# Optimization experiments

Hardware: AMD Instinct MI355X
Metric: run time of the kernel (lower is better)

The kernel has to match this reference:

```python
import jax, jax.numpy as jnp
import numpy as np

B = 32; N_NODES = 1000; WINDOW = 4; D = 128; N_PARTS = 10
T = 2; T_INT = 1; T_TEMP = 1
N_TOTAL = B * WINDOW * N_NODES
E_INT = 200000; E_TEMP = 96000


def setup_inputs() -> dict:
    key = jax.random.key(0)
    ks = jax.random.split(key, 24)
    inp = {}
    inp["node_inputs"] = jax.random.randint(ks[0], (B, N_NODES), 0, 10)
    inp["node_indices"] = jax.random.randint(ks[1], (E_INT,), 0, N_TOTAL)
    inp["neighbour_indices"] = jax.random.randint(ks[2], (E_INT,), 0, N_TOTAL)
    inp["temp_node_indices"] = jax.random.randint(ks[3], (E_TEMP,), 0, N_TOTAL)
    inp["temp_neighbour_indices"] = jax.random.randint(ks[4], (E_TEMP,), 0, N_TOTAL)

    def dense(k, din, dout):
        return jax.random.normal(k, (din, dout), jnp.float32) * np.float32(1.0 / np.sqrt(din))

    inp["embed_table"] = jax.random.normal(ks[5], (10, D), jnp.float32)
    # message MLP: 2*D -> 64 -> 64 -> 64 -> 64 -> D (4 gelu hidden, linear out)
    inp["msg_W_in"] = dense(ks[6], 2 * D, 64); inp["msg_b_in"] = jnp.zeros((64,), jnp.float32)
    inp["msg_W_hid"] = jax.random.normal(ks[7], (3, 64, 64), jnp.float32) * np.float32(1.0 / 8.0)
    inp["msg_b_hid"] = jnp.zeros((3, 64), jnp.float32)
    inp["msg_W_out"] = dense(ks[8], 64, D); inp["msg_b_out"] = jnp.zeros((D,), jnp.float32)
    # readout MLP: D -> 64 -> 64 -> 64 -> 64 -> n_parts
    inp["ro_W_in"] = dense(ks[9], D, 64); inp["ro_b_in"] = jnp.zeros((64,), jnp.float32)
    inp["ro_W_hid"] = jax.random.normal(ks[10], (3, 64, 64), jnp.float32) * np.float32(1.0 / 8.0)
    inp["ro_b_hid"] = jnp.zeros((3, 64), jnp.float32)
    inp["ro_W_out"] = dense(ks[11], 64, N_PARTS); inp["ro_b_out"] = jnp.zeros((N_PARTS,), jnp.float32)
    # GRU cells (tf.keras reset_after=True): kernel [D,3D], recurrent [D,3D], input+recurrent biases
    for nm, base in (("gi", 12), ("gt", 16)):
        inp[nm + "_Wx"] = dense(ks[base], D, 3 * D)
        inp[nm + "_Wh"] = dense(ks[base + 1], D, 3 * D)
        inp[nm + "_bi"] = jnp.zeros((3 * D,), jnp.float32)
        inp[nm + "_br"] = jnp.zeros((3 * D,), jnp.float32)
    return inp


def _mlp(x, W_in, b_in, W_hid, b_hid, W_out, b_out):
    h = jax.nn.gelu(x @ W_in + b_in, approximate=False)
    for i in range(W_hid.shape[0]):
        h = jax.nn.gelu(h @ W_hid[i] + b_hid[i], approximate=False)
    return h @ W_out + b_out


def _gru(h, x, Wx, Wh, bi, br):
    # tf.keras GRUCell, reset_after=True
    xz, xr, xh = jnp.split(x @ Wx + bi, 3, axis=1)
    hz, hr, hh = jnp.split(h @ Wh + br, 3, axis=1)
    z = jax.nn.sigmoid(xz + hz)
    r = jax.nn.sigmoid(xr + hr)
    cand = jnp.tanh(xh + r * hh)
    return z * h + (1.0 - z) * cand


def _message_mean(h, ni, bi, msg_p):
    g0 = h[ni]              # [E, D] node gather
    g1 = h[bi]              # [E, D] neighbour gather
    x = jnp.concatenate([jnp.concatenate([g0, g1], 1), jnp.concatenate([g1, g0], 1)], 0)  # [2E, 2D]
    msg = _mlp(x, *msg_p)   # [2E, D]
    seg = jnp.concatenate([bi, ni], 0)
    s = jax.ops.segment_sum(msg, seg, num_segments=h.shape[0])
    c = jax.ops.segment_sum(jnp.ones((seg.shape[0], 1), msg.dtype), seg, num_segments=h.shape[0])
    return s / jnp.maximum(c, 1.0)


def reference(node_inputs, node_indices, neighbour_indices, temp_node_indices, temp_neighbour_indices,
              embed_table, msg_W_in, msg_b_in, msg_W_hid, msg_b_hid, msg_W_out, msg_b_out,
              ro_W_in, ro_b_in, ro_W_hid, ro_b_hid, ro_W_out, ro_b_out,
              gi_Wx, gi_Wh, gi_bi, gi_br, gt_Wx, gt_Wh, gt_bi, gt_br):
    msg_p = (msg_W_in, msg_b_in, msg_W_hid, msg_b_hid, msg_W_out, msg_b_out)
    h = embed_table[node_inputs]                       # [B, N, D]
    h = jnp.repeat(h, WINDOW, axis=0).reshape(-1, D)   # [B*W*N, D]
    for _ in range(T):
        for _ in range(T_INT):
            m = _message_mean(h, node_indices, neighbour_indices, msg_p)
            h = _gru(h, m, gi_Wx, gi_Wh, gi_bi, gi_br)
        for _ in range(T_TEMP):
            m = _message_mean(h, temp_node_indices, temp_neighbour_indices, msg_p)
            h = _gru(h, m, gt_Wx, gt_Wh, gt_bi, gt_br)
    ridx = jnp.arange(N_NODES)[None, :] + jnp.arange(B)[:, None] * (WINDOW * N_NODES)
    return _mlp(h[ridx], ro_W_in, ro_b_in, ro_W_hid, ro_b_hid, ro_W_out, ro_b_out)  # [B, N, n_parts]
```

## Files before the change

### kernel.cpp

```cpp
#include <hip/hip_runtime.h>
#include <math.h>


#define DDIM 128
#define NTOT 128000
#define HBYTES 65536000ULL
#define EBLK 128

typedef unsigned short u16;
using f32x4 = __attribute__((ext_vector_type(4))) float;
using s16x8 = __attribute__((ext_vector_type(8))) short;

__device__ __forceinline__ float fast_rcp(float x) {
    return __builtin_amdgcn_rcpf(x);
}
__device__ __forceinline__ float gelu_fast(float x) {
    const float ax = fabsf(x) * 0.70710678118654752440f;
    const float t  = fast_rcp(1.0f + 0.3275911f * ax);
    const float poly = t * (0.254829592f + t * (-0.284496736f +
                       t * (1.421413741f + t * (-1.453152027f +
                       t * 1.061405429f))));
    const float e = __expf(-ax * ax);
    const float erfax = 1.0f - poly * e;
    const float erfv = copysignf(erfax, x);
    return 0.5f * x * (1.0f + erfv);
}
__device__ __forceinline__ float sigmoid_fast(float x) {
    return fast_rcp(1.0f + __expf(-x));
}
__device__ __forceinline__ float tanh_fast(float x) {
    const float e = __expf(2.0f * x);
    return 1.0f - 2.0f * fast_rcp(e + 1.0f);
}
__device__ __forceinline__ u16 f2bf(float x) {
    unsigned u = __float_as_uint(x);
    u += 0x7fffu + ((u >> 16) & 1u);
    return (u16)(u >> 16);
}
__device__ __forceinline__ float bf2f(u16 h) {
    return __uint_as_float(((unsigned)h) << 16);
}

__global__ __launch_bounds__(256) void embed_kernel(
    const int* __restrict__ inp, const float* __restrict__ table,
    float* __restrict__ h)
{
    int gid = blockIdx.x * 256 + threadIdx.x;
    if (gid >= NTOT * 32) return;
    int row = gid >> 5;
    int q   = gid & 31;
    int b   = row / 4000;
    int n   = (row % 4000) % 1000;
    int e   = inp[b * 1000 + n];
    ((float4*)h)[gid] = ((const float4*)table)[e * 32 + q];
}

__global__ __launch_bounds__(256) void hist_kernel(
    const int* __restrict__ ni, const int* __restrict__ bi, int E,
    int* __restrict__ deg)
{
    int g = blockIdx.x * 256 + threadIdx.x;
    if (g < E)          atomicAdd(&deg[bi[g]], 1);
    else if (g < 2 * E) atomicAdd(&deg[ni[g - E]], 1);
}

__global__ __launch_bounds__(256) void blockscan_kernel(
    const int* __restrict__ deg, int* __restrict__ offp, int* __restrict__ bsum)
{
    __shared__ int s[256];
    int tid = threadIdx.x;
    int i = blockIdx.x * 256 + tid;
    int v = deg[i];
    s[tid] = v;
    __syncthreads();
    for (int off = 1; off < 256; off <<= 1) {
        int t = (tid >= off) ? s[tid - off] : 0;
        __syncthreads();
        s[tid] += t;
        __syncthreads();
    }
    offp[i] = s[tid] - v;
    if (tid == 255) bsum[blockIdx.x] = s[255];
}

__global__ __launch_bounds__(512) void bscan_kernel(
    const int* __restrict__ bsum, int* __restrict__ bexc, int nb)
{
    __shared__ int s[512];
    int t = threadIdx.x;
    int v = (t < nb) ? bsum[t] : 0;
    s[t] = v;
    __syncthreads();
    for (int off = 1; off < 512; off <<= 1) {
        int u = (t >= off) ? s[t - off] : 0;
        __syncthreads();
        s[t] += u;
        __syncthreads();
    }
    if (t < nb) bexc[t] = s[t] - v;
}

__global__ __launch_bounds__(256) void fill_kernel(
    const int* __restrict__ ni, const int* __restrict__ bi, int E,
    const int* __restrict__ offp, const int* __restrict__ bexc,
    int* __restrict__ cursor, int* __restrict__ elist, int* __restrict__ slotseg)
{
    int g = blockIdx.x * 256 + threadIdx.x;
    if (g >= 2 * E) return;
    int seg = (g < E) ? bi[g] : ni[g - E];
    int pos = atomicAdd(&cursor[seg], 1);
    int slot = offp[seg] + bexc[seg >> 8] + pos;
    elist[slot] = g;
    slotseg[slot] = seg;
}

__global__ __launch_bounds__(256) void straddle_kernel(
    const int* __restrict__ slotseg, int nblocks32,
    int* __restrict__ list, int* __restrict__ count)
{
    int b = blockIdx.x * 256 + threadIdx.x + 1;
    if (b >= nblocks32) return;
    int s = slotseg[b * 32];
    if (s >= 0 && slotseg[b * 32 - 1] == s) {
        int pos = atomicAdd(count, 1);
        list[pos] = s;
    }
}

__global__ __launch_bounds__(64) void zero_rows_kernel(
    const int* __restrict__ list, const int* __restrict__ count,
    float* __restrict__ sbuf)
{
    int i = blockIdx.x;
    if (i >= *count) return;
    int seg = list[i];
    float4* row = (float4*)(sbuf + (size_t)seg * 64);
    if (threadIdx.x < 16) row[threadIdx.x] = make_float4(0.f, 0.f, 0.f, 0.f);
}

__global__ __launch_bounds__(256) void pack_gateB_kernel(
    const float* __restrict__ Wx, const float* __restrict__ Wh,
    u16* __restrict__ BH, u16* __restrict__ BL)
{
    int idx = blockIdx.x * 256 + threadIdx.x;
    if (idx >= 131072) return;
    int j    = idx & 7;
    int lane = (idx >> 3) & 63;
    int ntG  = (idx >> 9) & 31;
    int ktG  = idx >> 14;
    int k = ktG * 32 + (lane >> 4) * 8 + j;
    int n = ntG * 16 + (lane & 15);
    int g = n >> 7, jj = n & 127;
    float v;
    if (g == 0)      v = (k < 128) ? Wx[k * 384 + jj]       : Wh[(k - 128) * 384 + jj];
    else if (g == 1) v = (k < 128) ? Wx[k * 384 + 128 + jj] : Wh[(k - 128) * 384 + 128 + jj];
    else if (g == 2) v = (k < 128) ? Wx[k * 384 + 256 + jj] : 0.0f;
    else             v = (k < 128) ? 0.0f                   : Wh[(k - 128) * 384 + 256 + jj];
    u16 hb = f2bf(v);
    BH[idx] = hb;
    BL[idx] = f2bf(v - bf2f(hb));
}

__global__ __launch_bounds__(256) void pack_preB_kernel(
    const float* __restrict__ Win, u16* __restrict__ BH, u16* __restrict__ BL)
{
    int idx = blockIdx.x * 256 + threadIdx.x;
    if (idx >= 16384) return;
    int j    = idx & 7;
    int lane = (idx >> 3) & 63;
    int nt2  = (idx >> 9) & 7;
    int kt2  = idx >> 12;
    int k = kt2 * 32 + (lane >> 4) * 8 + j;
    int n = nt2 * 16 + (lane & 15);
    float v = (n < 64) ? Win[k * 64 + n] : Win[(128 + k) * 64 + (n - 64)];
    u16 hb = f2bf(v);
    BH[idx] = hb;
    BL[idx] = f2bf(v - bf2f(hb));
}

__global__ __launch_bounds__(256) void pack_hidB_kernel(
    const float* __restrict__ Whid, u16* __restrict__ BH, u16* __restrict__ BL)
{
    int idx = blockIdx.x * 256 + threadIdx.x;
    if (idx >= 12288) return;
    int j    = idx & 7;
    int lane = (idx >> 3) & 63;
    int nt   = (idx >> 9) & 3;
    int kt   = (idx >> 11) & 1;
    int L    = idx >> 12;
    int k = kt * 32 + (lane >> 4) * 8 + j;
    int n = nt * 16 + (lane & 15);
    float v = Whid[L * 4096 + k * 64 + n];
    u16 hb = f2bf(v);
    BH[idx] = hb;
    BL[idx] = f2bf(v - bf2f(hb));
}

__global__ __launch_bounds__(256) void pack_outB_kernel(
    const float* __restrict__ Wout, u16* __restrict__ BH, u16* __restrict__ BL)
{
    int idx = blockIdx.x * 256 + threadIdx.x;
    if (idx >= 8192) return;
    int j    = idx & 7;
    int lane = (idx >> 3) & 63;
    int nt   = (idx >> 9) & 7;
    int kt   = idx >> 12;
    int k = kt * 32 + (lane >> 4) * 8 + j;
    int n = nt * 16 + (lane & 15);
    float v = Wout[k * 128 + n];
    u16 hb = f2bf(v);
    BH[idx] = hb;
    BL[idx] = f2bf(v - bf2f(hb));
}

__global__ __launch_bounds__(512, 2) void node_pre_mfma(
    const float* __restrict__ h,
    const u16* __restrict__ BpH, const u16* __restrict__ BpL,
    const float* __restrict__ binp, float* __restrict__ pout)
{
    __shared__ short sm[32768];
    const int tid  = threadIdx.x;
    const int lane = tid & 63;
    const int w    = tid >> 6;
    const int jg   = w & 1;
    const int mh   = w >> 1;
    const int nbase = blockIdx.x * 128;

    const int mS = tid >> 2, q = tid & 3;
    const int nodeS = nbase + mS;
    const int laneS = (mS & 15) + 16 * q;
    const int seg_m = mS >> 4;

    #pragma unroll
    for (int c = 0; c < 4; ++c) {
        const int kl = c * 32 + q * 8;
        const float* src = h + (size_t)nodeS * DDIM + kl;
        const float4 v0 = ((const float4*)src)[0];
        const float4 v1 = ((const float4*)src)[1];
        float xv[8] = { v0.x, v0.y, v0.z, v0.w, v1.x, v1.y, v1.z, v1.w };
        s16x8 hi8, lo8;
        #pragma unroll
        for (int i = 0; i < 8; ++i) {
            u16 hb = f2bf(xv[i]);
            hi8[i] = (short)hb;
            lo8[i] = (short)f2bf(xv[i] - bf2f(hb));
        }
        const int off = (c * 8 + seg_m) * 512 + laneS * 8;
        *(s16x8*)(sm + off)         = hi8;
        *(s16x8*)(sm + off + 16384) = lo8;
    }
    __syncthreads();

    f32x4 acc2[2][4];
    #pragma unroll
    for (int mf = 0; mf < 2; ++mf)
        #pragma unroll
        for (int t4 = 0; t4 < 4; ++t4)
            acc2[mf][t4] = (f32x4){0.f, 0.f, 0.f, 0.f};

    const s16x8* Ph8 = (const s16x8*)BpH;
    const s16x8* Pl8 = (const s16x8*)BpL;
    #pragma unroll
    for (int kt2 = 0; kt2 < 4; ++kt2) {
        const int a0off = (kt2 * 8 + 2 * mh) * 512 + lane * 8;
        const s16x8 aH0 = *(const s16x8*)(sm + a0off);
        const s16x8 aL0 = *(const s16x8*)(sm + 16384 + a0off);
        const s16x8 aH1 = *(const s16x8*)(sm + a0off + 512);
        const s16x8 aL1 = *(const s16x8*)(sm + 16384 + a0off + 512);
        #pragma unroll
        for (int t4 = 0; t4 < 4; ++t4) {
            const int idx = (kt2 * 8 + jg * 4 + t4) * 64 + lane;
            const s16x8 bH = Ph8[idx];
            const s16x8 bL = Pl8[idx];
            acc2[0][t4] = __builtin_amdgcn_mfma_f32_16x16x32_bf16(aH0, bH, acc2[0][t4], 0, 0, 0);
            acc2[0][t4] = __builtin_amdgcn_mfma_f32_16x16x32_bf16(aH0, bL, acc2[0][t4], 0, 0, 0);
            acc2[0][t4] = __builtin_amdgcn_mfma_f32_16x16x32_bf16(aL0, bH, acc2[0][t4], 0, 0, 0);
            acc2[1][t4] = __builtin_amdgcn_mfma_f32_16x16x32_bf16(aH1, bH, acc2[1][t4], 0, 0, 0);
            acc2[1][t4] = __builtin_amdgcn_mfma_f32_16x16x32_bf16(aH1, bL, acc2[1][t4], 0, 0, 0);
            acc2[1][t4] = __builtin_amdgcn_mfma_f32_16x16x32_bf16(aL1, bH, acc2[1][t4], 0, 0, 0);
        }
    }
    #pragma unroll
    for (int mf = 0; mf < 2; ++mf) {
        const int mtile = 2 * mh + mf;
        #pragma unroll
        for (int t4 = 0; t4 < 4; ++t4) {
            const int n = jg * 64 + t4 * 16 + (lane & 15);
            const float badd = (n < 64) ? binp[n] : 0.0f;
            #pragma unroll
            for (int r = 0; r < 4; ++r) {
                const int m = mtile * 16 + (lane >> 4) * 4 + r;
                pout[(size_t)(nbase + m) * DDIM + n] = acc2[mf][t4][r] + badd;
            }
        }
    }
}

__global__ __launch_bounds__(512) void edge_mlp_mfma(
    const int* __restrict__ ni, const int* __restrict__ bi, int E,
    const int* __restrict__ elist, const int* __restrict__ slotseg,
    const float* __restrict__ p,
    const u16* __restrict__ BhH, const u16* __restrict__ BhL,
    const float* __restrict__ bhid,
    float* __restrict__ sbuf)
{
    __shared__ short smA[17408];
    __shared__ int   segLDS[EBLK];
    __shared__ int   segedge[2];
    float* scat = (float*)smA;

    const int tid  = threadIdx.x;
    const int lane = tid & 63;
    const int w    = tid >> 6;
    const int s0   = blockIdx.x * EBLK;

    if (tid < 128) segLDS[tid] = slotseg[s0 + tid];
    if (tid == 0) segedge[0] = slotseg[s0 - 1];
    if (tid == 1) segedge[1] = slotseg[s0 + EBLK];

    {
        const int m  = (tid & 15) | (w << 4);
        const int gg = (tid >> 4) & 3;
        const int slot = s0 + m;
        const int g = elist[slot];
        int first, second;
        if (g < E) { first = ni[g];     second = bi[g];     }
        else       { first = bi[g - E]; second = ni[g - E]; }
        #pragma unroll
        for (int kt = 0; kt < 2; ++kt) {
            const int k0 = kt * 32 + gg * 8;
            const float4* pa = (const float4*)(p + (size_t)first  * DDIM + k0);
            const float4* pb = (const float4*)(p + (size_t)second * DDIM + 64 + k0);
            const float4 a0 = pa[0], a1 = pa[1], b0 = pb[0], b1 = pb[1];
            float x[8] = { a0.x + b0.x, a0.y + b0.y, a0.z + b0.z, a0.w + b0.w,
                           a1.x + b1.x, a1.y + b1.y, a1.z + b1.z, a1.w + b1.w };
            s16x8 hi8, lo8;
            #pragma unroll
            for (int j = 0; j < 8; ++j) {
                const float v = gelu_fast(x[j]);
                u16 hb = f2bf(v);
                hi8[j] = (short)hb;
                lo8[j] = (short)f2bf(v - bf2f(hb));
            }
            const int off = (kt * 8 + w) * 512 + lane * 8;
            *(s16x8*)(smA + off)        = hi8;
            *(s16x8*)(smA + 8192 + off) = lo8;
        }
    }

    const int mt = w;
    for (int L = 0; L < 2; ++L) {
        f32x4 acc[4];
        #pragma unroll
        for (int nt = 0; nt < 4; ++nt) {
            const float bv = bhid[L * 64 + nt * 16 + (lane & 15)];
            acc[nt] = (f32x4){bv, bv, bv, bv};
        }
        #pragma unroll
        for (int kt = 0; kt < 2; ++kt) {
            const s16x8 aH = *(const s16x8*)(smA + (kt * 8 + mt) * 512 + lane * 8);
            const s16x8 aL = *(const s16x8*)(smA + 8192 + (kt * 8 + mt) * 512 + lane * 8);
            #pragma unroll
            for (int nt = 0; nt < 4; ++nt) {
                const int bidx = (L * 8 + kt * 4 + nt) * 64 + lane;
                const s16x8 bH = ((const s16x8*)BhH)[bidx];
                const s16x8 bL = ((const s16x8*)BhL)[bidx];
                acc[nt] = __builtin_amdgcn_mfma_f32_16x16x32_bf16(aH, bH, acc[nt], 0, 0, 0);
                acc[nt] = __builtin_amdgcn_mfma_f32_16x16x32_bf16(aH, bL, acc[nt], 0, 0, 0);
                acc[nt] = __builtin_amdgcn_mfma_f32_16x16x32_bf16(aL, bH, acc[nt], 0, 0, 0);
            }
        }
        #pragma unroll
        for (int nt = 0; nt < 4; ++nt) {
            #pragma unroll
            for (int r = 0; r < 4; ++r) {
                const float v = gelu_fast(acc[nt][r]);
                const int ml  = (lane >> 4) * 4 + r;
                const int k   = nt * 16 + (lane & 15);
                const int kt2 = k >> 5, gg = (k >> 3) & 3, j = k & 7;
                const int off = (kt2 * 8 + mt) * 512 + (ml + 16 * gg) * 8 + j;
                u16 hb = f2bf(v);
                smA[off]        = (short)hb;
                smA[8192 + off] = (short)f2bf(v - bf2f(hb));
            }
        }
    }

    float gl[4][4];
    {
        f32x4 acc[4];
        #pragma unroll
        for (int nt = 0; nt < 4; ++nt) {
            const float bv = bhid[2 * 64 + nt * 16 + (lane & 15)];
            acc[nt] = (f32x4){bv, bv, bv, bv};
        }
        #pragma unroll
        for (int kt = 0; kt < 2; ++kt) {
            const s16x8 aH = *(const s16x8*)(smA + (kt * 8 + mt) * 512 + lane * 8);
            const s16x8 aL = *(const s16x8*)(smA + 8192 + (kt * 8 + mt) * 512 + lane * 8);
            #pragma unroll
            for (int nt = 0; nt < 4; ++nt) {
                const int bidx = (2 * 8 + kt * 4 + nt) * 64 + lane;
                const s16x8 bH = ((const s16x8*)BhH)[bidx];
                const s16x8 bL = ((const s16x8*)BhL)[bidx];
                acc[nt] = __builtin_amdgcn_mfma_f32_16x16x32_bf16(aH, bH, acc[nt], 0, 0, 0);
                acc[nt] = __builtin_amdgcn_mfma_f32_16x16x32_bf16(aH, bL, acc[nt], 0, 0, 0);
                acc[nt] = __builtin_amdgcn_mfma_f32_16x16x32_bf16(aL, bH, acc[nt], 0, 0, 0);
            }
        }
        #pragma unroll
        for (int nt = 0; nt < 4; ++nt)
            #pragma unroll
            for (int r = 0; r < 4; ++r)
                gl[nt][r] = gelu_fast(acc[nt][r]);
    }

    __syncthreads();
    #pragma unroll
    for (int nt = 0; nt < 4; ++nt)
        #pragma unroll
        for (int r = 0; r < 4; ++r)
            scat[(mt * 16 + (lane >> 4) * 4 + r) * 68 + nt * 16 + (lane & 15)]
                = gl[nt][r];
    __syncthreads();

    if (tid < 256) {
        const int col = tid & 63;
        const int r0  = (tid >> 6) * 32;
        const int r1  = r0 + 32;
        int   runSeg = -2;
        float runacc = 0.0f;
        bool  leftC  = true;
        for (int rowi = r0; rowi < r1; ++rowi) {
            const int sg = segLDS[rowi];
            const float v = scat[rowi * 68 + col];
            if (sg != runSeg) {
                if (runSeg >= 0) {
                    float* pp = sbuf + (size_t)runSeg * 64 + col;
                    if (leftC) *pp = runacc;
                    else       atomicAdd(pp, runacc);
                }
                runSeg = sg;
                runacc = v;
                if (rowi == r0) {
                    const int prev = (rowi == 0) ? segedge[0] : segLDS[rowi - 1];
                    leftC = (prev != sg);
                } else {
                    leftC = true;
                }
            } else {
                runacc += v;
            }
        }
        if (runSeg >= 0) {
            const int nxt = (r1 == 128) ? segedge[1] : segLDS[r1];
            const bool rightC = (nxt != runSeg);
            float* pp = sbuf + (size_t)runSeg * 64 + col;
            if (leftC && rightC) *pp = runacc;
            else                 atomicAdd(pp, runacc);
        }
    }
}

__global__ __launch_bounds__(256, 3) void gru_mfma_kernel(
    float* __restrict__ hio, const float* __restrict__ Ssum,
    const int* __restrict__ deg,
    const u16* __restrict__ WoH, const u16* __restrict__ WoL,
    const float* __restrict__ bo,
    const u16* __restrict__ BgH, const u16* __restrict__ BgL,
    const float* __restrict__ bi_, const float* __restrict__ br_,
    const u16* __restrict__ BpH, const u16* __restrict__ BpL,
    const float* __restrict__ binp,
    float* __restrict__ pout)
{
    __shared__ short sm[16384];
    const int tid  = threadIdx.x;
    const int lane = tid & 63;
    const int w    = tid >> 6;
    const int jg   = w & 1;
    const int mh   = w >> 1;
    const int nbase = blockIdx.x * 64;

    const int mS = tid >> 2, q = tid & 3;
    const int nodeS = nbase + mS;
    const int laneS = (mS & 15) + 16 * q;
    const int seg_m = mS >> 4;
    const int dg = deg[nodeS];
    const float ci = (dg > 0) ? fast_rcp((float)dg) : 0.0f;

    #pragma unroll
    for (int c = 0; c < 2; ++c) {
        const int kl = c * 32 + q * 8;
        const float* src = Ssum + (size_t)nodeS * 64 + kl;
        const float4 v0 = ((const float4*)src)[0];
        const float4 v1 = ((const float4*)src)[1];
        float xv[8] = { v0.x * ci, v0.y * ci, v0.z * ci, v0.w * ci,
                        v1.x * ci, v1.y * ci, v1.z * ci, v1.w * ci };
        s16x8 hi8, lo8;
        #pragma unroll
        for (int i = 0; i < 8; ++i) {
            u16 hb = f2bf(xv[i]);
            hi8[i] = (short)hb;
            lo8[i] = (short)f2bf(xv[i] - bf2f(hb));
        }
        const int off = (c * 4 + seg_m) * 512 + laneS * 8;
        *(s16x8*)(sm + off)        = hi8;
        *(s16x8*)(sm + off + 8192) = lo8;
    }
    __syncthreads();

    f32x4 am[2][4];
    #pragma unroll
    for (int mf = 0; mf < 2; ++mf)
        #pragma unroll
        for (int t4 = 0; t4 < 4; ++t4)
            am[mf][t4] = (f32x4){0.f, 0.f, 0.f, 0.f};
    {
        const s16x8* WH8 = (const s16x8*)WoH;
        const s16x8* WL8 = (const s16x8*)WoL;
        #pragma unroll
        for (int kt = 0; kt < 2; ++kt) {
            const int a0off = (kt * 4 + 2 * mh) * 512 + lane * 8;
            const s16x8 aH0 = *(const s16x8*)(sm + a0off);
            const s16x8 aL0 = *(const s16x8*)(sm + 8192 + a0off);
            const s16x8 aH1 = *(const s16x8*)(sm + a0off + 512);
            const s16x8 aL1 = *(const s16x8*)(sm + 8192 + a0off + 512);
            #pragma unroll
            for (int t4 = 0; t4 < 4; ++t4) {
                const int idx = (kt * 8 + jg * 4 + t4) * 64 + lane;
                const s16x8 bH = WH8[idx];
                const s16x8 bL = WL8[idx];
                am[0][t4] = __builtin_amdgcn_mfma_f32_16x16x32_bf16(aH0, bH, am[0][t4], 0, 0, 0);
                am[0][t4] = __builtin_amdgcn_mfma_f32_16x16x32_bf16(aH0, bL, am[0][t4], 0, 0, 0);
                am[0][t4] = __builtin_amdgcn_mfma_f32_16x16x32_bf16(aL0, bH, am[0][t4], 0, 0, 0);
                am[1][t4] = __builtin_amdgcn_mfma_f32_16x16x32_bf16(aH1, bH, am[1][t4], 0, 0, 0);
                am[1][t4] = __builtin_amdgcn_mfma_f32_16x16x32_bf16(aH1, bL, am[1][t4], 0, 0, 0);
                am[1][t4] = __builtin_amdgcn_mfma_f32_16x16x32_bf16(aL1, bH, am[1][t4], 0, 0, 0);
            }
        }
    }
    __syncthreads();

    {
        bool bon[2][4];
        #pragma unroll
        for (int mf = 0; mf < 2; ++mf)
            #pragma unroll
            for (int r = 0; r < 4; ++r)
                bon[mf][r] = deg[nbase + (2 * mh + mf) * 16 + (lane >> 4) * 4 + r] > 0;
        #pragma unroll
        for (int t4 = 0; t4 < 4; ++t4) {
            const int n = jg * 64 + t4 * 16 + (lane & 15);
            const float bv = bo[n];
            const int kt2 = n >> 5, gg = (n >> 3) & 3, jj = n & 7;
            #pragma unroll
            for (int mf = 0; mf < 2; ++mf) {
                const int mtile = 2 * mh + mf;
                #pragma unroll
                for (int r = 0; r < 4; ++r) {
                    const int m15 = (lane >> 4) * 4 + r;
                    const float mv = am[mf][t4][r] + (bon[mf][r] ? bv : 0.0f);
                    const int off = (kt2 * 4 + mtile) * 512 + (m15 + 16 * gg) * 8 + jj;
                    u16 hb = f2bf(mv);
                    sm[off]        = (short)hb;
                    sm[off + 8192] = (short)f2bf(mv - bf2f(hb));
                }
            }
        }
    }
    __syncthreads();

    f32x4 acc[2][4][4];
    #pragma unroll
    for (int mf = 0; mf < 2; ++mf)
        #pragma unroll
        for (int g = 0; g < 4; ++g)
            #pragma unroll
            for (int t4 = 0; t4 < 4; ++t4)
                acc[mf][g][t4] = (f32x4){0.f, 0.f, 0.f, 0.f};

    const s16x8* Bh8 = (const s16x8*)BgH;
    const s16x8* Bl8 = (const s16x8*)BgL;
    #pragma unroll
    for (int kt = 0; kt < 4; ++kt) {
        const int a0off = (kt * 4 + 2 * mh) * 512 + lane * 8;
        const s16x8 aH0 = *(const s16x8*)(sm + a0off);
        const s16x8 aL0 = *(const s16x8*)(sm + 8192 + a0off);
        const s16x8 aH1 = *(const s16x8*)(sm + a0off + 512);
        const s16x8 aL1 = *(const s16x8*)(sm + 8192 + a0off + 512);
        #pragma unroll
        for (int g = 0; g < 3; ++g) {
            #pragma unroll
            for (int t4 = 0; t4 < 4; ++t4) {
                const int idx = (kt * 32 + g * 8 + jg * 4 + t4) * 64 + lane;
                const s16x8 bH = Bh8[idx];
                const s16x8 bL = Bl8[idx];
                acc[0][g][t4] = __builtin_amdgcn_mfma_f32_16x16x32_bf16(aH0, bH, acc[0][g][t4], 0, 0, 0);
                acc[0][g][t4] = __builtin_amdgcn_mfma_f32_16x16x32_bf16(aH0, bL, acc[0][g][t4], 0, 0, 0);
                acc[0][g][t4] = __builtin_amdgcn_mfma_f32_16x16x32_bf16(aL0, bH, acc[0][g][t4], 0, 0, 0);
                acc[1][g][t4] = __builtin_amdgcn_mfma_f32_16x16x32_bf16(aH1, bH, acc[1][g][t4], 0, 0, 0);
                acc[1][g][t4] = __builtin_amdgcn_mfma_f32_16x16x32_bf16(aH1, bL, acc[1][g][t4], 0, 0, 0);
                acc[1][g][t4] = __builtin_amdgcn_mfma_f32_16x16x32_bf16(aL1, bH, acc[1][g][t4], 0, 0, 0);
            }
        }
    }
    __syncthreads();

    #pragma unroll
    for (int c = 0; c < 4; ++c) {
        const int kl = c * 32 + q * 8;
        const float* src = hio + (size_t)nodeS * DDIM + kl;
        const float4 v0 = ((const float4*)src)[0];
        const float4 v1 = ((const float4*)src)[1];
        float xv[8] = { v0.x, v0.y, v0.z, v0.w, v1.x, v1.y, v1.z, v1.w };
        s16x8 hi8, lo8;
        #pragma unroll
        for (int i = 0; i < 8; ++i) {
            u16 hb = f2bf(xv[i]);
            hi8[i] = (short)hb;
            lo8[i] = (short)f2bf(xv[i] - bf2f(hb));
        }
        const int off = (c * 4 + seg_m) * 512 + laneS * 8;
        *(s16x8*)(sm + off)        = hi8;
        *(s16x8*)(sm + off + 8192) = lo8;
    }
    __syncthreads();

    #pragma unroll
    for (int kt = 0; kt < 4; ++kt) {
        const int ktG = 4 + kt;
        const int a0off = (kt * 4 + 2 * mh) * 512 + lane * 8;
        const s16x8 aH0 = *(const s16x8*)(sm + a0off);
        const s16x8 aL0 = *(const s16x8*)(sm + 8192 + a0off);
        const s16x8 aH1 = *(const s16x8*)(sm + a0off + 512);
        const s16x8 aL1 = *(const s16x8*)(sm + 8192 + a0off + 512);
        #pragma unroll
        for (int gi = 0; gi < 3; ++gi) {
            const int g = (gi == 2) ? 3 : gi;
            #pragma unroll
            for (int t4 = 0; t4 < 4; ++t4) {
                const int idx = (ktG * 32 + g * 8 + jg * 4 + t4) * 64 + lane;
                const s16x8 bH = Bh8[idx];
                const s16x8 bL = Bl8[idx];
                acc[0][g][t4] = __builtin_amdgcn_mfma_f32_16x16x32_bf16(aH0, bH, acc[0][g][t4], 0, 0, 0);
                acc[0][g][t4] = __builtin_amdgcn_mfma_f32_16x16x32_bf16(aH0, bL, acc[0][g][t4], 0, 0, 0);
                acc[0][g][t4] = __builtin_amdgcn_mfma_f32_16x16x32_bf16(aL0, bH, acc[0][g][t4], 0, 0, 0);
                acc[1][g][t4] = __builtin_amdgcn_mfma_f32_16x16x32_bf16(aH1, bH, acc[1][g][t4], 0, 0, 0);
                acc[1][g][t4] = __builtin_amdgcn_mfma_f32_16x16x32_bf16(aH1, bL, acc[1][g][t4], 0, 0, 0);
                acc[1][g][t4] = __builtin_amdgcn_mfma_f32_16x16x32_bf16(aL1, bH, acc[1][g][t4], 0, 0, 0);
            }
        }
    }

    float hn[2][4][4];
    #pragma unroll
    for (int t4 = 0; t4 < 4; ++t4) {
        const int j = jg * 64 + t4 * 16 + (lane & 15);
        const float b_az = bi_[j]       + br_[j];
        const float b_ar = bi_[128 + j] + br_[128 + j];
        const float b_xh = bi_[256 + j];
        const float b_hh = br_[256 + j];
        const int jbase = (j >> 5) * 2048 + ((j >> 3) & 3) * 128 + (j & 7);
        #pragma unroll
        for (int mf = 0; mf < 2; ++mf) {
            const int mtile = 2 * mh + mf;
            #pragma unroll
            for (int r = 0; r < 4; ++r) {
                const int m15 = (lane >> 4) * 4 + r;
                const int off = jbase + mtile * 512 + m15 * 8;
                const float hv = bf2f((u16)sm[off]) + bf2f((u16)sm[8192 + off]);
                const int m = mtile * 16 + m15;
                const float az = acc[mf][0][t4][r] + b_az;
                const float ar = acc[mf][1][t4][r] + b_ar;
                const float xh = acc[mf][2][t4][r] + b_xh;
                const float hh = acc[mf][3][t4][r] + b_hh;
                const float z    = sigmoid_fast(az);
                const float rr   = sigmoid_fast(ar);
                const float cand = tanh_fast(xh + rr * hh);
                const float v    = z * hv + (1.0f - z) * cand;
                hio[(size_t)(nbase + m) * DDIM + j] = v;
                hn[mf][t4][r] = v;
            }
        }
    }
    __syncthreads();

    #pragma unroll
    for (int mf = 0; mf < 2; ++mf) {
        const int mtile = 2 * mh + mf;
        #pragma unroll
        for (int t4 = 0; t4 < 4; ++t4) {
            #pragma unroll
            for (int r = 0; r < 4; ++r) {
                const int m15 = (lane >> 4) * 4 + r;
                const int j   = jg * 64 + t4 * 16 + (lane & 15);
                const int kt2 = j >> 5, gg = (j >> 3) & 3, jj = j & 7;
                const int off = (kt2 * 4 + mtile) * 512 + (m15 + 16 * gg) * 8 + jj;
                const float v = hn[mf][t4][r];
                u16 hb = f2bf(v);
                sm[off]        = (short)hb;
                sm[off + 8192] = (short)f2bf(v - bf2f(hb));
            }
        }
    }
    __syncthreads();

    f32x4 acc2[2][4];
    #pragma unroll
    for (int mf = 0; mf < 2; ++mf)
        #pragma unroll
        for (int t4 = 0; t4 < 4; ++t4)
            acc2[mf][t4] = (f32x4){0.f, 0.f, 0.f, 0.f};

    const s16x8* Ph8 = (const s16x8*)BpH;
    const s16x8* Pl8 = (const s16x8*)BpL;
    #pragma unroll
    for (int kt2 = 0; kt2 < 4; ++kt2) {
        const int a0off = (kt2 * 4 + 2 * mh) * 512 + lane * 8;
        const s16x8 aH0 = *(const s16x8*)(sm + a0off);
        const s16x8 aL0 = *(const s16x8*)(sm + 8192 + a0off);
        const s16x8 aH1 = *(const s16x8*)(sm + a0off + 512);
        const s16x8 aL1 = *(const s16x8*)(sm + 8192 + a0off + 512);
        #pragma unroll
        for (int t4 = 0; t4 < 4; ++t4) {
            const int idx = (kt2 * 8 + jg * 4 + t4) * 64 + lane;
            const s16x8 bH = Ph8[idx];
            const s16x8 bL = Pl8[idx];
            acc2[0][t4] = __builtin_amdgcn_mfma_f32_16x16x32_bf16(aH0, bH, acc2[0][t4], 0, 0, 0);
            acc2[0][t4] = __builtin_amdgcn_mfma_f32_16x16x32_bf16(aH0, bL, acc2[0][t4], 0, 0, 0);
            acc2[0][t4] = __builtin_amdgcn_mfma_f32_16x16x32_bf16(aL0, bH, acc2[0][t4], 0, 0, 0);
            acc2[1][t4] = __builtin_amdgcn_mfma_f32_16x16x32_bf16(aH1, bH, acc2[1][t4], 0, 0, 0);
            acc2[1][t4] = __builtin_amdgcn_mfma_f32_16x16x32_bf16(aH1, bL, acc2[1][t4], 0, 0, 0);
            acc2[1][t4] = __builtin_amdgcn_mfma_f32_16x16x32_bf16(aL1, bH, acc2[1][t4], 0, 0, 0);
        }
    }
    #pragma unroll
    for (int mf = 0; mf < 2; ++mf) {
        const int mtile = 2 * mh + mf;
        #pragma unroll
        for (int t4 = 0; t4 < 4; ++t4) {
            const int n = jg * 64 + t4 * 16 + (lane & 15);
            const float badd = (n < 64) ? binp[n] : 0.0f;
            #pragma unroll
            for (int r = 0; r < 4; ++r) {
                const int m = mtile * 16 + (lane >> 4) * 4 + r;
                pout[(size_t)(nbase + m) * DDIM + n] = acc2[mf][t4][r] + badd;
            }
        }
    }
}

__global__ __launch_bounds__(64) void readout_kernel(
    const float* __restrict__ h,
    const float* __restrict__ Win,  const float* __restrict__ bin,
    const float* __restrict__ Whid, const float* __restrict__ bhid,
    const float* __restrict__ Wout, const float* __restrict__ bout,
    float* __restrict__ out)
{
    __shared__ float xs[64 * 65];
    const int tid = threadIdx.x;
    const int row = blockIdx.x * 64 + tid;
    const int b = row / 1000, n = row % 1000;
    const float4* xrow = (const float4*)(h + ((size_t)b * 4000 + n) * DDIM);

    {
        float acc[64];
        #pragma unroll
        for (int j = 0; j < 64; ++j) acc[j] = bin[j];
        #pragma unroll 2
        for (int k4 = 0; k4 < 32; ++k4) {
            float4 xv = xrow[k4];
            #pragma unroll
            for (int kk = 0; kk < 4; ++kk) {
                const float xk = (&xv.x)[kk];
                const float* wr = Win + (size_t)(k4 * 4 + kk) * 64;
                #pragma unroll
                for (int j = 0; j < 64; ++j) acc[j] = fmaf(xk, wr[j], acc[j]);
            }
        }
        #pragma unroll
        for (int j = 0; j < 64; ++j) xs[tid * 65 + j] = gelu_fast(acc[j]);
    }

    for (int L = 0; L < 3; ++L) {
        float acc[64];
        #pragma unroll
        for (int j = 0; j < 64; ++j) acc[j] = bhid[L * 64 + j];
        #pragma unroll 4
        for (int k = 0; k < 64; ++k) {
            const float xk = xs[tid * 65 + k];
            const float* wr = Whid + (size_t)L * 4096 + (size_t)k * 64;
            #pragma unroll
            for (int j = 0; j < 64; ++j) acc[j] = fmaf(xk, wr[j], acc[j]);
        }
        #pragma unroll
        for (int j = 0; j < 64; ++j) xs[tid * 65 + j] = gelu_fast(acc[j]);
    }

    float acc[10];
    #pragma unroll
    for (int pj = 0; pj < 10; ++pj) acc[pj] = bout[pj];
    #pragma unroll 4
    for (int k = 0; k < 64; ++k) {
        const float xk = xs[tid * 65 + k];
        const float* wr = Wout + k * 10;
        #pragma unroll
        for (int pj = 0; pj < 10; ++pj) acc[pj] = fmaf(xk, wr[pj], acc[pj]);
    }
    #pragma unroll
    for (int pj = 0; pj < 10; ++pj) out[(size_t)row * 10 + pj] = acc[pj];
}

extern "C" void kernel_launch(void* const* d_in, const int* in_sizes, int n_in,
                              void* d_out, int out_size, void* d_ws, size_t ws_size,
                              hipStream_t stream) {
    const int*   node_inputs = (const int*)d_in[0];
    const int*   ni_int = (const int*)d_in[1];
    const int*   bi_int = (const int*)d_in[2];
    const int*   ni_tmp = (const int*)d_in[3];
    const int*   bi_tmp = (const int*)d_in[4];
    const float* embed  = (const float*)d_in[5];
    const float* mWin   = (const float*)d_in[6];
    const float* mbin   = (const float*)d_in[7];
    const float* mWhid  = (const float*)d_in[8];
    const float* mbhid  = (const float*)d_in[9];
    const float* mWout  = (const float*)d_in[10];
    const float* mbout  = (const float*)d_in[11];
    const float* roWin  = (const float*)d_in[12];
    const float* robin  = (const float*)d_in[13];
    const float* roWhid = (const float*)d_in[14];
    const float* robhid = (const float*)d_in[15];
    const float* roWout = (const float*)d_in[16];
    const float* robout = (const float*)d_in[17];
    const float* giWx = (const float*)d_in[18];
    const float* giWh = (const float*)d_in[19];
    const float* gibi = (const float*)d_in[20];
    const float* gibr = (const float*)d_in[21];
    const float* gtWx = (const float*)d_in[22];
    const float* gtWh = (const float*)d_in[23];
    const float* gtbi = (const float*)d_in[24];
    const float* gtbr = (const float*)d_in[25];
    float* out = (float*)d_out;

    const int E_INT = 200000, E_TMP = 96000;
    const int NSLOT_I = 400000;
    const int NSLOT_T = 192000;
    const int NBLK_I = NSLOT_I / EBLK;
    const int NBLK_T = NSLOT_T / EBLK;
    const int NS32_I = NSLOT_I / 32;
    const int NS32_T = NSLOT_T / 32;

    char* ws = (char*)d_ws;
    float* B0 = (float*)(ws);
    float* B1 = (float*)(ws + HBYTES);
    float* B2 = (float*)(ws + 2 * HBYTES);
    char*  ib = ws + 3 * HBYTES;

    int* deg_i   = (int*)(ib);
    int* deg_t   = (int*)(ib + 512000);
    int* offp_i  = (int*)(ib + 1024000);
    int* offp_t  = (int*)(ib + 1536000);
    int* bexc_i  = (int*)(ib + 2048000);
    int* bexc_t  = (int*)(ib + 2052096);
    int* bsum    = (int*)(ib + 2056192);
    int* cursor  = (int*)(ib + 2060288);
    int* el_i    = (int*)(ib + 2572288);
    int* el_t    = (int*)(ib + 4172288);
    int* ssi_raw = (int*)(ib + 4940288);
    int* sst_raw = (int*)(ib + 6540296);
    char* fb = ib + 8114176;
    u16* BgiH = (u16*)(fb);
    u16* BgiL = (u16*)(fb +  262144);
    u16* BgtH = (u16*)(fb +  524288);
    u16* BgtL = (u16*)(fb +  786432);
    u16* BpH  = (u16*)(fb + 1048576);
    u16* BpL  = (u16*)(fb + 1081344);
    u16* EhH  = (u16*)(fb + 1114112);
    u16* EhL  = (u16*)(fb + 1138688);
    u16* EoH  = (u16*)(fb + 1163264);
    u16* EoL  = (u16*)(fb + 1179648);
    int* str_i  = (int*)(fb + 1196032);
    int* str_t  = (int*)(fb + 1246032);
    int* strc_i = (int*)(fb + 1270032);
    int* strc_t = (int*)(fb + 1270036);
    int* ssi = ssi_raw + 1;
    int* sst = sst_raw + 1;

    embed_kernel<<<16000, 256, 0, stream>>>(node_inputs, embed, B0);

    hipMemsetAsync(deg_i, 0, NTOT * sizeof(int), stream);
    hipMemsetAsync(deg_t, 0, NTOT * sizeof(int), stream);
    hist_kernel<<<(2 * E_INT + 255) / 256, 256, 0, stream>>>(ni_int, bi_int, E_INT, deg_i);
    hist_kernel<<<(2 * E_TMP + 255) / 256, 256, 0, stream>>>(ni_tmp, bi_tmp, E_TMP, deg_t);

    hipMemsetAsync(ssi_raw, 0xFF, (size_t)(NSLOT_I + 2) * sizeof(int), stream);
    hipMemsetAsync(sst_raw, 0xFF, (size_t)(NSLOT_T + 2) * sizeof(int), stream);

    blockscan_kernel<<<500, 256, 0, stream>>>(deg_i, offp_i, bsum);
    bscan_kernel<<<1, 512, 0, stream>>>(bsum, bexc_i, 500);
    hipMemsetAsync(cursor, 0, NTOT * sizeof(int), stream);
    fill_kernel<<<(2 * E_INT + 255) / 256, 256, 0, stream>>>(
        ni_int, bi_int, E_INT, offp_i, bexc_i, cursor, el_i, ssi);

    blockscan_kernel<<<500, 256, 0, stream>>>(deg_t, offp_t, bsum);
    bscan_kernel<<<1, 512, 0, stream>>>(bsum, bexc_t, 500);
    hipMemsetAsync(cursor, 0, NTOT * sizeof(int), stream);
    fill_kernel<<<(2 * E_TMP + 255) / 256, 256, 0, stream>>>(
        ni_tmp, bi_tmp, E_TMP, offp_t, bexc_t, cursor, el_t, sst);

    hipMemsetAsync(strc_i, 0, sizeof(int), stream);
    hipMemsetAsync(strc_t, 0, sizeof(int), stream);
    straddle_kernel<<<(NS32_I + 255) / 256, 256, 0, stream>>>(ssi, NS32_I, str_i, strc_i);
    straddle_kernel<<<(NS32_T + 255) / 256, 256, 0, stream>>>(sst, NS32_T, str_t, strc_t);

    pack_gateB_kernel<<<512, 256, 0, stream>>>(giWx, giWh, BgiH, BgiL);
    pack_gateB_kernel<<<512, 256, 0, stream>>>(gtWx, gtWh, BgtH, BgtL);
    pack_preB_kernel<<<64, 256, 0, stream>>>(mWin, BpH, BpL);
    pack_hidB_kernel<<<48, 256, 0, stream>>>(mWhid, EhH, EhL);
    pack_outB_kernel<<<32, 256, 0, stream>>>(mWout, EoH, EoL);

    node_pre_mfma<<<NTOT / 128, 512, 0, stream>>>(B0, BpH, BpL, mbin, B1);

    for (int ph = 0; ph < 4; ++ph) {
        const bool isInt = (ph % 2 == 0);
        if (isInt) {
            zero_rows_kernel<<<NS32_I, 64, 0, stream>>>(str_i, strc_i, B2);
            edge_mlp_mfma<<<NBLK_I, 512, 0, stream>>>(
                ni_int, bi_int, E_INT, el_i, ssi, B1,
                EhH, EhL, mbhid, B2);
            gru_mfma_kernel<<<NTOT / 64, 256, 0, stream>>>(
                B0, B2, deg_i, EoH, EoL, mbout,
                BgiH, BgiL, gibi, gibr, BpH, BpL, mbin, B1);
        } else {
            zero_rows_kernel<<<NS32_T, 64, 0, stream>>>(str_t, strc_t, B2);
            edge_mlp_mfma<<<NBLK_T, 512, 0, stream>>>(
                ni_tmp, bi_tmp, E_TMP, el_t, sst, B1,
                EhH, EhL, mbhid, B2);
            gru_mfma_kernel<<<NTOT / 64, 256, 0, stream>>>(
                B0, B2, deg_t, EoH, EoL, mbout,
                BgtH, BgtL, gtbi, gtbr, BpH, BpL, mbin, B1);
        }
    }

    readout_kernel<<<500, 64, 0, stream>>>(
        B0, roWin, robin, roWhid, robhid, roWout, robout, out);
}
```

Measured before the change: 1.376 ms.

## Fold message output projection into GRU input weights to skip intermediate GEMM

```diff
diff --git a/kernel.cpp b/kernel.cpp
--- a/kernel.cpp
+++ b/kernel.cpp
@@ -138,27 +138,58 @@
     if (threadIdx.x < 16) row[threadIdx.x] = make_float4(0.f, 0.f, 0.f, 0.f);
 }
 
-__global__ __launch_bounds__(256) void pack_gateB_kernel(
-    const float* __restrict__ Wx, const float* __restrict__ Wh,
+
+__global__ __launch_bounds__(256) void pack_gateBx_kernel(
+    const float* __restrict__ Wout, const float* __restrict__ Wx,
     u16* __restrict__ BH, u16* __restrict__ BL)
 {
     int idx = blockIdx.x * 256 + threadIdx.x;
-    if (idx >= 131072) return;
+    if (idx >= 24576) return;
     int j    = idx & 7;
     int lane = (idx >> 3) & 63;
-    int ntG  = (idx >> 9) & 31;
-    int ktG  = idx >> 14;
-    int k = ktG * 32 + (lane >> 4) * 8 + j;
-    int n = ntG * 16 + (lane & 15);
-    int g = n >> 7, jj = n & 127;
-    float v;
-    if (g == 0)      v = (k < 128) ? Wx[k * 384 + jj]       : Wh[(k - 128) * 384 + jj];
-    else if (g == 1) v = (k < 128) ? Wx[k * 384 + 128 + jj] : Wh[(k - 128) * 384 + 128 + jj];
-    else if (g == 2) v = (k < 128) ? Wx[k * 384 + 256 + jj] : 0.0f;
-    else             v = (k < 128) ? 0.0f                   : Wh[(k - 128) * 384 + 256 + jj];
+    int tile = idx >> 9;
+    int nt   = tile & 7;
+    int g    = (tile >> 3) % 3;
+    int kt   = tile / 24;
+    int k   = kt * 32 + (lane >> 4) * 8 + j;
+    int col = g * 128 + nt * 16 + (lane & 15);
+    float acc = 0.0f;
+    for (int t = 0; t < 128; ++t)
+        acc = fmaf(Wout[k * 128 + t], Wx[t * 384 + col], acc);
+    u16 hb = f2bf(acc);
+    BH[idx] = hb;
+    BL[idx] = f2bf(acc - bf2f(hb));
+}
+
+__global__ __launch_bounds__(256) void pack_gateBh_kernel(
+    const float* __restrict__ Wh, u16* __restrict__ BH, u16* __restrict__ BL)
+{
+    int idx = blockIdx.x * 256 + threadIdx.x;
+    if (idx >= 49152) return;
+    int j    = idx & 7;
+    int lane = (idx >> 3) & 63;
+    int tile = idx >> 9;
+    int nt   = tile & 7;
+    int s    = (tile >> 3) % 3;
+    int kt   = tile / 24;
+    int k    = kt * 32 + (lane >> 4) * 8 + j;
+    int col  = ((s == 2) ? 256 : s * 128) + nt * 16 + (lane & 15);
+    float v = Wh[k * 384 + col];
     u16 hb = f2bf(v);
     BH[idx] = hb;
     BL[idx] = f2bf(v - bf2f(hb));
+}
+
+__global__ __launch_bounds__(256) void pack_gbias_kernel(
+    const float* __restrict__ bout, const float* __restrict__ Wx,
+    float* __restrict__ bc)
+{
+    int n = blockIdx.x * 256 + threadIdx.x;
+    if (n >= 384) return;
+    float acc = 0.0f;
+    for (int t = 0; t < 128; ++t)
+        acc = fmaf(bout[t], Wx[t * 384 + n], acc);
+    bc[n] = acc;
 }
 
 __global__ __launch_bounds__(256) void pack_preB_kernel(
@@ -191,23 +222,6 @@
     int k = kt * 32 + (lane >> 4) * 8 + j;
     int n = nt * 16 + (lane & 15);
     float v = Whid[L * 4096 + k * 64 + n];
-    u16 hb = f2bf(v);
-    BH[idx] = hb;
-    BL[idx] = f2bf(v - bf2f(hb));
-}
-
-__global__ __launch_bounds__(256) void pack_outB_kernel(
-    const float* __restrict__ Wout, u16* __restrict__ BH, u16* __restrict__ BL)
-{
-    int idx = blockIdx.x * 256 + threadIdx.x;
-    if (idx >= 8192) return;
-    int j    = idx & 7;
-    int lane = (idx >> 3) & 63;
-    int nt   = (idx >> 9) & 7;
-    int kt   = idx >> 12;
-    int k = kt * 32 + (lane >> 4) * 8 + j;
-    int n = nt * 16 + (lane & 15);
-    float v = Wout[k * 128 + n];
     u16 hb = f2bf(v);
     BH[idx] = hb;
     BL[idx] = f2bf(v - bf2f(hb));
@@ -465,9 +479,9 @@
 __global__ __launch_bounds__(256, 3) void gru_mfma_kernel(
     float* __restrict__ hio, const float* __restrict__ Ssum,
     const int* __restrict__ deg,
-    const u16* __restrict__ WoH, const u16* __restrict__ WoL,
-    const float* __restrict__ bo,
-    const u16* __restrict__ BgH, const u16* __restrict__ BgL,
+    const u16* __restrict__ BxH, const u16* __restrict__ BxL,
+    const u16* __restrict__ BhH, const u16* __restrict__ BhL,
+    const float* __restrict__ bc,
     const float* __restrict__ bi_, const float* __restrict__ br_,
     const u16* __restrict__ BpH, const u16* __restrict__ BpL,
     const float* __restrict__ binp,
@@ -509,15 +523,18 @@
     }
     __syncthreads();
 
-    f32x4 am[2][4];
+    f32x4 acc[2][4][4];
     #pragma unroll
     for (int mf = 0; mf < 2; ++mf)
         #pragma unroll
-        for (int t4 = 0; t4 < 4; ++t4)
-            am[mf][t4] = (f32x4){0.f, 0.f, 0.f, 0.f};
+        for (int g = 0; g < 4; ++g)
+            #pragma unroll
+            for (int t4 = 0; t4 < 4; ++t4)
+                acc[mf][g][t4] = (f32x4){0.f, 0.f, 0.f, 0.f};
+
     {
-        const s16x8* WH8 = (const s16x8*)WoH;
-        const s16x8* WL8 = (const s16x8*)WoL;
+        const s16x8* Bx8 = (const s16x8*)BxH;
+        const s16x8* Bxl8 = (const s16x8*)BxL;
         #pragma unroll
         for (int kt = 0; kt < 2; ++kt) {
             const int a0off = (kt * 4 + 2 * mh) * 512 + lane * 8;
@@ -526,81 +543,19 @@
             const s16x8 aH1 = *(const s16x8*)(sm + a0off + 512);
             const s16x8 aL1 = *(const s16x8*)(sm + 8192 + a0off + 512);
             #pragma unroll
-            for (int t4 = 0; t4 < 4; ++t4) {
-                const int idx = (kt * 8 + jg * 4 + t4) * 64 + lane;
-                const s16x8 bH = WH8[idx];
-                const s16x8 bL = WL8[idx];
-                am[0][t4] = __builtin_amdgcn_mfma_f32_16x16x32_bf16(aH0, bH, am[0][t4], 0, 0, 0);
-                am[0][t4] = __builtin_amdgcn_mfma_f32_16x16x32_bf16(aH0, bL, am[0][t4], 0, 0, 0);
-                am[0][t4] = __builtin_amdgcn_mfma_f32_16x16x32_bf16(aL0, bH, am[0][t4], 0, 0, 0);
-                am[1][t4] = __builtin_amdgcn_mfma_f32_16x16x32_bf16(aH1, bH, am[1][t4], 0, 0, 0);
-                am[1][t4] = __builtin_amdgcn_mfma_f32_16x16x32_bf16(aH1, bL, am[1][t4], 0, 0, 0);
-                am[1][t4] = __builtin_amdgcn_mfma_f32_16x16x32_bf16(aL1, bH, am[1][t4], 0, 0, 0);
-            }
-        }
-    }
-    __syncthreads();
-
-    {
-        bool bon[2][4];
-        #pragma unroll
-        for (int mf = 0; mf < 2; ++mf)
-            #pragma unroll
-            for (int r = 0; r < 4; ++r)
-                bon[mf][r] = deg[nbase + (2 * mh + mf) * 16 + (lane >> 4) * 4 + r] > 0;
-        #pragma unroll
-        for (int t4 = 0; t4 < 4; ++t4) {
-            const int n = jg * 64 + t4 * 16 + (lane & 15);
-            const float bv = bo[n];
-            const int kt2 = n >> 5, gg = (n >> 3) & 3, jj = n & 7;
-            #pragma unroll
-            for (int mf = 0; mf < 2; ++mf) {
-                const int mtile = 2 * mh + mf;
+            for (int g = 0; g < 3; ++g) {
                 #pragma unroll
-                for (int r = 0; r < 4; ++r) {
-                    const int m15 = (lane >> 4) * 4 + r;
-                    const float mv = am[mf][t4][r] + (bon[mf][r] ? bv : 0.0f);
-                    const int off = (kt2 * 4 + mtile) * 512 + (m15 + 16 * gg) * 8 + jj;
-                    u16 hb = f2bf(mv);
-                    sm[off]        = (short)hb;
-                    sm[off + 8192] = (short)f2bf(mv - bf2f(hb));
+                for (int t4 = 0; t4 < 4; ++t4) {
+                    const int idx = (kt * 24 + g * 8 + jg * 4 + t4) * 64 + lane;
+                    const s16x8 bH = Bx8[idx];
+                    const s16x8 bL = Bxl8[idx];
+                    acc[0][g][t4] = __builtin_amdgcn_mfma_f32_16x16x32_bf16(aH0, bH, acc[0][g][t4], 0, 0, 0);
+                    acc[0][g][t4] = __builtin_amdgcn_mfma_f32_16x16x32_bf16(aH0, bL, acc[0][g][t4], 0, 0, 0);
+                    acc[0][g][t4] = __builtin_amdgcn_mfma_f32_16x16x32_bf16(aL0, bH, acc[0][g][t4], 0, 0, 0);
+                    acc[1][g][t4] = __builtin_amdgcn_mfma_f32_16x16x32_bf16(aH1, bH, acc[1][g][t4], 0, 0, 0);
+                    acc[1][g][t4] = __builtin_amdgcn_mfma_f32_16x16x32_bf16(aH1, bL, acc[1][g][t4], 0, 0, 0);
+                    acc[1][g][t4] = __builtin_amdgcn_mfma_f32_16x16x32_bf16(aL1, bH, acc[1][g][t4], 0, 0, 0);
                 }
-            }
-        }
-    }
-    __syncthreads();
-
-    f32x4 acc[2][4][4];
-    #pragma unroll
-    for (int mf = 0; mf < 2; ++mf)
-        #pragma unroll
-        for (int g = 0; g < 4; ++g)
-            #pragma unroll
-            for (int t4 = 0; t4 < 4; ++t4)
-                acc[mf][g][t4] = (f32x4){0.f, 0.f, 0.f, 0.f};
-
-    const s16x8* Bh8 = (const s16x8*)BgH;
-    const s16x8* Bl8 = (const s16x8*)BgL;
-    #pragma unroll
-    for (int kt = 0; kt < 4; ++kt) {
-        const int a0off = (kt * 4 + 2 * mh) * 512 + lane * 8;
-        const s16x8 aH0 = *(const s16x8*)(sm + a0off);
-        const s16x8 aL0 = *(const s16x8*)(sm + 8192 + a0off);
-        const s16x8 aH1 = *(const s16x8*)(sm + a0off + 512);
-        const s16x8 aL1 = *(const s16x8*)(sm + 8192 + a0off + 512);
-        #pragma unroll
-        for (int g = 0; g < 3; ++g) {
-            #pragma unroll
-            for (int t4 = 0; t4 < 4; ++t4) {
-                const int idx = (kt * 32 + g * 8 + jg * 4 + t4) * 64 + lane;
-                const s16x8 bH = Bh8[idx];
-                const s16x8 bL = Bl8[idx];
-                acc[0][g][t4] = __builtin_amdgcn_mfma_f32_16x16x32_bf16(aH0, bH, acc[0][g][t4], 0, 0, 0);
-                acc[0][g][t4] = __builtin_amdgcn_mfma_f32_16x16x32_bf16(aH0, bL, acc[0][g][t4], 0, 0, 0);
-                acc[0][g][t4] = __builtin_amdgcn_mfma_f32_16x16x32_bf16(aL0, bH, acc[0][g][t4], 0, 0, 0);
-                acc[1][g][t4] = __builtin_amdgcn_mfma_f32_16x16x32_bf16(aH1, bH, acc[1][g][t4], 0, 0, 0);
-                acc[1][g][t4] = __builtin_amdgcn_mfma_f32_16x16x32_bf16(aH1, bL, acc[1][g][t4], 0, 0, 0);
-                acc[1][g][t4] = __builtin_amdgcn_mfma_f32_16x16x32_bf16(aL1, bH, acc[1][g][t4], 0, 0, 0);
             }
         }
     }
@@ -626,31 +581,41 @@
     }
     __syncthreads();
 
-    #pragma unroll
-    for (int kt = 0; kt < 4; ++kt) {
-        const int ktG = 4 + kt;
-        const int a0off = (kt * 4 + 2 * mh) * 512 + lane * 8;
-        const s16x8 aH0 = *(const s16x8*)(sm + a0off);
-        const s16x8 aL0 = *(const s16x8*)(sm + 8192 + a0off);
-        const s16x8 aH1 = *(const s16x8*)(sm + a0off + 512);
-        const s16x8 aL1 = *(const s16x8*)(sm + 8192 + a0off + 512);
-        #pragma unroll
-        for (int gi = 0; gi < 3; ++gi) {
-            const int g = (gi == 2) ? 3 : gi;
-            #pragma unroll
-            for (int t4 = 0; t4 < 4; ++t4) {
-                const int idx = (ktG * 32 + g * 8 + jg * 4 + t4) * 64 + lane;
-                const s16x8 bH = Bh8[idx];
-                const s16x8 bL = Bl8[idx];
-                acc[0][g][t4] = __builtin_amdgcn_mfma_f32_16x16x32_bf16(aH0, bH, acc[0][g][t4], 0, 0, 0);
-                acc[0][g][t4] = __builtin_amdgcn_mfma_f32_16x16x32_bf16(aH0, bL, acc[0][g][t4], 0, 0, 0);
-                acc[0][g][t4] = __builtin_amdgcn_mfma_f32_16x16x32_bf16(aL0, bH, acc[0][g][t4], 0, 0, 0);
-                acc[1][g][t4] = __builtin_amdgcn_mfma_f32_16x16x32_bf16(aH1, bH, acc[1][g][t4], 0, 0, 0);
-                acc[1][g][t4] = __builtin_amdgcn_mfma_f32_16x16x32_bf16(aH1, bL, acc[1][g][t4], 0, 0, 0);
-                acc[1][g][t4] = __builtin_amdgcn_mfma_f32_16x16x32_bf16(aL1, bH, acc[1][g][t4], 0, 0, 0);
-            }
-        }
-    }
+    {
+        const s16x8* Bh8 = (const s16x8*)BhH;
+        const s16x8* Bhl8 = (const s16x8*)BhL;
+        #pragma unroll
+        for (int kt = 0; kt < 4; ++kt) {
+            const int a0off = (kt * 4 + 2 * mh) * 512 + lane * 8;
+            const s16x8 aH0 = *(const s16x8*)(sm + a0off);
+            const s16x8 aL0 = *(const s16x8*)(sm + 8192 + a0off);
+            const s16x8 aH1 = *(const s16x8*)(sm + a0off + 512);
+            const s16x8 aL1 = *(const s16x8*)(sm + 8192 + a0off + 512);
+            #pragma unroll
+            for (int s = 0; s < 3; ++s) {
+                const int g = (s == 2) ? 3 : s;
+                #pragma unroll
+                for (int t4 = 0; t4 < 4; ++t4) {
+                    const int idx = (kt * 24 + s * 8 + jg * 4 + t4) * 64 + lane;
+                    const s16x8 bH = Bh8[idx];
+                    const s16x8 bL = Bhl8[idx];
+                    acc[0][g][t4] = __builtin_amdgcn_mfma_f32_16x16x32_bf16(aH0, bH, acc[0][g][t4], 0, 0, 0);
+                    acc[0][g][t4] = __builtin_amdgcn_mfma_f32_16x16x32_bf16(aH0, bL, acc[0][g][t4], 0, 0, 0);
+                    acc[0][g][t4] = __builtin_amdgcn_mfma_f32_16x16x32_bf16(aL0, bH, acc[0][g][t4], 0, 0, 0);
+                    acc[1][g][t4] = __builtin_amdgcn_mfma_f32_16x16x32_bf16(aH1, bH, acc[1][g][t4], 0, 0, 0);
+                    acc[1][g][t4] = __builtin_amdgcn_mfma_f32_16x16x32_bf16(aH1, bL, acc[1][g][t4], 0, 0, 0);
+                    acc[1][g][t4] = __builtin_amdgcn_mfma_f32_16x16x32_bf16(aL1, bH, acc[1][g][t4], 0, 0, 0);
+                }
+            }
+        }
+    }
+
+    bool bon[2][4];
+    #pragma unroll
+    for (int mf = 0; mf < 2; ++mf)
+        #pragma unroll
+        for (int r = 0; r < 4; ++r)
+            bon[mf][r] = deg[nbase + (2 * mh + mf) * 16 + (lane >> 4) * 4 + r] > 0;
 
     float hn[2][4][4];
     #pragma unroll
@@ -660,6 +625,9 @@
         const float b_ar = bi_[128 + j] + br_[128 + j];
         const float b_xh = bi_[256 + j];
         const float b_hh = br_[256 + j];
+        const float bcz = bc[j];
+        const float bcr = bc[128 + j];
+        const float bcx = bc[256 + j];
         const int jbase = (j >> 5) * 2048 + ((j >> 3) & 3) * 128 + (j & 7);
         #pragma unroll
         for (int mf = 0; mf < 2; ++mf) {
@@ -670,9 +638,10 @@
                 const int off = jbase + mtile * 512 + m15 * 8;
                 const float hv = bf2f((u16)sm[off]) + bf2f((u16)sm[8192 + off]);
                 const int m = mtile * 16 + m15;
-                const float az = acc[mf][0][t4][r] + b_az;
-                const float ar = acc[mf][1][t4][r] + b_ar;
-                const float xh = acc[mf][2][t4][r] + b_xh;
+                const float bsel = bon[mf][r] ? 1.0f : 0.0f;
+                const float az = acc[mf][0][t4][r] + b_az + bsel * bcz;
+                const float ar = acc[mf][1][t4][r] + b_ar + bsel * bcr;
+                const float xh = acc[mf][2][t4][r] + b_xh + bsel * bcx;
                 const float hh = acc[mf][3][t4][r] + b_hh;
                 const float z    = sigmoid_fast(az);
                 const float rr   = sigmoid_fast(ar);
@@ -869,20 +838,24 @@
     int* ssi_raw = (int*)(ib + 4940288);
     int* sst_raw = (int*)(ib + 6540296);
     char* fb = ib + 8114176;
-    u16* BgiH = (u16*)(fb);
-    u16* BgiL = (u16*)(fb +  262144);
-    u16* BgtH = (u16*)(fb +  524288);
-    u16* BgtL = (u16*)(fb +  786432);
-    u16* BpH  = (u16*)(fb + 1048576);
-    u16* BpL  = (u16*)(fb + 1081344);
-    u16* EhH  = (u16*)(fb + 1114112);
-    u16* EhL  = (u16*)(fb + 1138688);
-    u16* EoH  = (u16*)(fb + 1163264);
-    u16* EoL  = (u16*)(fb + 1179648);
-    int* str_i  = (int*)(fb + 1196032);
-    int* str_t  = (int*)(fb + 1246032);
-    int* strc_i = (int*)(fb + 1270032);
-    int* strc_t = (int*)(fb + 1270036);
+    u16* BxiH = (u16*)(fb);
+    u16* BxiL = (u16*)(fb +  49152);
+    u16* BhiH = (u16*)(fb +  98304);
+    u16* BhiL = (u16*)(fb + 196608);
+    u16* BxtH = (u16*)(fb + 294912);
+    u16* BxtL = (u16*)(fb + 344064);
+    u16* BhtH = (u16*)(fb + 393216);
+    u16* BhtL = (u16*)(fb + 491520);
+    float* bci = (float*)(fb + 589824);
+    float* bct = (float*)(fb + 591360);
+    u16* BpH  = (u16*)(fb + 592896);
+    u16* BpL  = (u16*)(fb + 625664);
+    u16* EhH  = (u16*)(fb + 658432);
+    u16* EhL  = (u16*)(fb + 683008);
+    int* str_i  = (int*)(fb + 707584);
+    int* str_t  = (int*)(fb + 757584);
+    int* strc_i = (int*)(fb + 781584);
+    int* strc_t = (int*)(fb + 781588);
     int* ssi = ssi_raw + 1;
     int* sst = sst_raw + 1;
 
@@ -913,11 +886,14 @@
     straddle_kernel<<<(NS32_I + 255) / 256, 256, 0, stream>>>(ssi, NS32_I, str_i, strc_i);
     straddle_kernel<<<(NS32_T + 255) / 256, 256, 0, stream>>>(sst, NS32_T, str_t, strc_t);
 
-    pack_gateB_kernel<<<512, 256, 0, stream>>>(giWx, giWh, BgiH, BgiL);
-    pack_gateB_kernel<<<512, 256, 0, stream>>>(gtWx, gtWh, BgtH, BgtL);
+    pack_gateBx_kernel<<<96, 256, 0, stream>>>(mWout, giWx, BxiH, BxiL);
+    pack_gateBx_kernel<<<96, 256, 0, stream>>>(mWout, gtWx, BxtH, BxtL);
+    pack_gateBh_kernel<<<192, 256, 0, stream>>>(giWh, BhiH, BhiL);
+    pack_gateBh_kernel<<<192, 256, 0, stream>>>(gtWh, BhtH, BhtL);
+    pack_gbias_kernel<<<2, 256, 0, stream>>>(mbout, giWx, bci);
+    pack_gbias_kernel<<<2, 256, 0, stream>>>(mbout, gtWx, bct);
     pack_preB_kernel<<<64, 256, 0, stream>>>(mWin, BpH, BpL);
     pack_hidB_kernel<<<48, 256, 0, stream>>>(mWhid, EhH, EhL);
-    pack_outB_kernel<<<32, 256, 0, stream>>>(mWout, EoH, EoL);
 
     node_pre_mfma<<<NTOT / 128, 512, 0, stream>>>(B0, BpH, BpL, mbin, B1);
 
@@ -929,16 +905,16 @@
                 ni_int, bi_int, E_INT, el_i, ssi, B1,
                 EhH, EhL, mbhid, B2);
             gru_mfma_kernel<<<NTOT / 64, 256, 0, stream>>>(
-                B0, B2, deg_i, EoH, EoL, mbout,
-                BgiH, BgiL, gibi, gibr, BpH, BpL, mbin, B1);
+                B0, B2, deg_i, BxiH, BxiL, BhiH, BhiL, bci,
+                gibi, gibr, BpH, BpL, mbin, B1);
         } else {
             zero_rows_kernel<<<NS32_T, 64, 0, stream>>>(str_t, strc_t, B2);
             edge_mlp_mfma<<<NBLK_T, 512, 0, stream>>>(
                 ni_tmp, bi_tmp, E_TMP, el_t, sst, B1,
                 EhH, EhL, mbhid, B2);
             gru_mfma_kernel<<<NTOT / 64, 256, 0, stream>>>(
-                B0, B2, deg_t, EoH, EoL, mbout,
-                BgtH, BgtL, gtbi, gtbr, BpH, BpL, mbin, B1);
+                B0, B2, deg_t, BxtH, BxtL, BhtH, BhtL, bct,
+                gtbi, gtbr, BpH, BpL, mbin, B1);
         }
     }
 
```

After: 1.253 ms, median of 2. 8.9% less time.
